# Performance work log

Hardware: AMD Instinct MI355X
Metric: run time of the kernel (lower is better)

Reference implementation:

```python
import jax, jax.numpy as jnp
import numpy as np

# static config matching init_kwargs / input_specs
SPATIAL = [(64, 64), (32, 32), (16, 16), (8, 8)]  # (H_l, W_l) per level
LEN = sum(h * w for h, w in SPATIAL)  # 5440
B, C, H, L, P = 4, 256, 8, 4, 4
DH = C // H
DFF = 1024
EPS = 1e-5


def layer_norm(x, g, b):
    m = x.mean(-1, keepdims=True)
    v = ((x - m) ** 2).mean(-1, keepdims=True)
    return (x - m) / jnp.sqrt(v + EPS) * g + b


def msda_core(value, sampling_locations, attn_weights):
    """Multi-scale deformable attention core (bilinear sample + weighted sum).
    value: [B, Len, H, DH]; sampling_locations: [B, Lq, H, L, P, 2] in [0,1];
    attn_weights: [B, Lq, H, L, P]. Returns [B, Lq, C].
    Matches grid_sample(bilinear, align_corners=False, padding_mode='zeros')."""
    Bn, Lq = sampling_locations.shape[0], sampling_locations.shape[1]
    out = jnp.zeros((Bn, H, Lq, DH), value.dtype)
    start = 0
    for l, (Hl, Wl) in enumerate(SPATIAL):
        vl = value[:, start:start + Hl * Wl]          # [B, Hl*Wl, H, DH]
        start += Hl * Wl
        vl = vl.transpose(0, 2, 1, 3)                  # [B, H, Hl*Wl, DH]
        loc = sampling_locations[:, :, :, l].transpose(0, 2, 1, 3, 4)  # [B,H,Lq,P,2]
        # align_corners=False: pixel = loc * size - 0.5
        px = loc[..., 0] * Wl - 0.5
        py = loc[..., 1] * Hl - 0.5
        x0 = jnp.floor(px); y0 = jnp.floor(py)
        wx1 = px - x0; wy1 = py - y0
        x0i = x0.astype(jnp.int32); y0i = y0.astype(jnp.int32)
        samp = jnp.zeros((Bn, H, Lq, P, DH), value.dtype)
        for dx, dy in ((0, 0), (1, 0), (0, 1), (1, 1)):
            ix = x0i + dx; iy = y0i + dy
            w = (wx1 if dx else 1.0 - wx1) * (wy1 if dy else 1.0 - wy1)
            valid = (ix >= 0) & (ix < Wl) & (iy >= 0) & (iy < Hl)
            idx = jnp.clip(iy, 0, Hl - 1) * Wl + jnp.clip(ix, 0, Wl - 1)  # [B,H,Lq,P]
            g = jnp.take_along_axis(vl, idx.reshape(Bn, H, -1)[..., None], axis=2)
            g = g.reshape(Bn, H, Lq, P, DH)
            samp = samp + g * (w * valid)[..., None]
        aw = attn_weights[:, :, :, l].transpose(0, 2, 1, 3)  # [B,H,Lq,P]
        out = out + (samp * aw[..., None]).sum(3)
    return out.transpose(0, 2, 1, 3).reshape(Bn, Lq, C)


def setup_inputs() -> dict:
    key = jax.random.key(0)
    ks = jax.random.split(key, 20)
    inp = {
        'src': jax.random.normal(ks[0], (B, LEN, C), jnp.float32),
        'pos': jax.random.normal(ks[1], (B, LEN, C), jnp.float32),
        'reference_points': jax.random.uniform(ks[2], (B, LEN, L, 2), jnp.float32),
        'spatial_shapes': jnp.array(SPATIAL, dtype=jnp.int32),
        'level_start_index': jnp.array(np.cumsum([0] + [h * w for h, w in SPATIAL[:-1]]), dtype=jnp.int32),
        'valid_ratios': jnp.ones((B, L, 2), jnp.float32),
        # MSDeformAttn params
        'w_off': jax.random.normal(ks[3], (C, H * L * P * 2), jnp.float32) * 0.01,
        'b_off': jax.random.normal(ks[4], (H * L * P * 2,), jnp.float32) * 0.5,
        'w_attn': jax.random.normal(ks[5], (C, H * L * P), jnp.float32) * 0.05,
        'b_attn': jnp.zeros((H * L * P,), jnp.float32),
        'w_val': jax.random.normal(ks[6], (C, C), jnp.float32) * 0.05,
        'b_val': jnp.zeros((C,), jnp.float32),
        'w_out': jax.random.normal(ks[7], (C, C), jnp.float32) * 0.05,
        'b_out': jnp.zeros((C,), jnp.float32),
        # norm1 + FFN + norm2 params
        'g1': jnp.ones((C,), jnp.float32), 'be1': jnp.zeros((C,), jnp.float32),
        'w1': jax.random.normal(ks[8], (C, DFF), jnp.float32) * 0.05,
        'b1': jnp.zeros((DFF,), jnp.float32),
        'w2': jax.random.normal(ks[9], (DFF, C), jnp.float32) * 0.05,
        'b2': jnp.zeros((C,), jnp.float32),
        'g2': jnp.ones((C,), jnp.float32), 'be2': jnp.zeros((C,), jnp.float32),
    }
    return inp


def reference(src, pos, reference_points, spatial_shapes, level_start_index, valid_ratios,
              w_off, b_off, w_attn, b_attn, w_val, b_val, w_out, b_out,
              g1, be1, w1, b1, w2, b2, g2, be2):
    Bn, Lq, _ = src.shape
    q = src + pos  # with_pos_embed
    off = (q @ w_off + b_off).reshape(Bn, Lq, H, L, P, 2)
    aw = jax.nn.softmax((q @ w_attn + b_attn).reshape(Bn, Lq, H, L * P), axis=-1)
    aw = aw.reshape(Bn, Lq, H, L, P)
    # offset normalizer is (W_l, H_l) per level
    norm = jnp.array([[w, h] for h, w in SPATIAL], dtype=src.dtype)  # [L, 2]
    loc = reference_points[:, :, None, :, None, :] + off / norm[None, None, None, :, None, :]
    value = (src @ w_val + b_val).reshape(Bn, Lq, H, DH)  # padding_mask is None
    attn_out = msda_core(value, loc, aw) @ w_out + b_out
    x = layer_norm(src + attn_out, g1, be1)
    ffn = jax.nn.relu(x @ w1 + b1) @ w2 + b2
    return layer_norm(x + ffn, g2, be2)
```

## Files before the change

### kernel.cpp

```cpp
#include <hip/hip_runtime.h>
#include <hip/hip_fp16.h>
#include <math.h>

#define LEN   5440
#define NTOK  21760
#define DFF   1024
#define LEPS  1e-5f

typedef __attribute__((ext_vector_type(8))) _Float16 f16x8;
typedef __attribute__((ext_vector_type(4))) float f32x4;

__device__ __forceinline__ float4 f4_add(float4 a, float4 b) {
    return make_float4(a.x + b.x, a.y + b.y, a.z + b.z, a.w + b.w);
}

__device__ __forceinline__ __half2 u2h2(unsigned u) {
    union { unsigned u; __half2 h; } c; c.u = u; return c.h;
}

__device__ __forceinline__ int swz8(int lin, int nwg) {
    const int q = nwg >> 3, r = nwg & 7;
    const int x = lin & 7, j = lin >> 3;
    return (x < r ? x * (q + 1) : r * (q + 1) + (x - r) * q) + j;
}

__global__ __launch_bounds__(256) void pack_k(const float* __restrict__ w_off,
                                              const float* __restrict__ w_attn,
                                              const float* __restrict__ w_val,
                                              const float* __restrict__ b_off,
                                              const float* __restrict__ b_attn,
                                              const float* __restrict__ b_val,
                                              const float* __restrict__ w_out,
                                              const float* __restrict__ w1,
                                              const float* __restrict__ w2,
                                              __half* __restrict__ WcatT,
                                              __half* __restrict__ woutT,
                                              __half* __restrict__ w1T,
                                              __half* __restrict__ w2T,
                                              float* __restrict__ bcat) {
    const int i = blockIdx.x * 256 + threadIdx.x;
    if (i < 163840) {
        const int c = i >> 8, k = i & 255;
        float v;
        if (c < 256)      v = w_off[k * 256 + c];
        else if (c < 384) v = w_attn[k * 128 + (c - 256)];
        else              v = w_val[k * 256 + (c - 384)];
        WcatT[i] = __float2half(v);
    } else if (i < 229376) {
        const int j = i - 163840, c = j >> 8, k = j & 255;
        woutT[j] = __float2half(w_out[k * 256 + c]);
    } else if (i < 491520) {
        const int j = i - 229376, c = j >> 8, k = j & 255;
        w1T[j] = __float2half(w1[k * 1024 + c]);
    } else if (i < 753664) {
        const int j = i - 491520, c = j >> 10, k = j & 1023;
        w2T[j] = __float2half(w2[k * 256 + c]);
    }
    if (i < 640) {
        bcat[i] = (i < 256) ? b_off[i] : (i < 384) ? b_attn[i - 256] : b_val[i - 384];
    }
}

template <bool AF32, int OMODE>
__global__ __launch_bounds__(256) void hgemm_k(const void* __restrict__ Ap,
                                               const float* __restrict__ A2f,
                                               const __half* __restrict__ Bt,
                                               const float* __restrict__ bias,
                                               float* __restrict__ Cf,
                                               __half* __restrict__ Ch,
                                               int NnF, int NnH, int K, int colSwitch) {
    __shared__ __half As[128][40];
    __shared__ __half Bs[128][40];
    const int nbx = gridDim.x;
    const int nwg = nbx * gridDim.y;
    const int tile = swz8(blockIdx.y * nbx + blockIdx.x, nwg);
    const int bx = tile % nbx, by = tile / nbx;

    const int tid = threadIdx.x;
    const int lane = tid & 63;
    const int wave = tid >> 6;
    const int wr = (wave >> 1) * 64;
    const int wc = (wave & 1) * 64;
    const bool useA2 = AF32 && (bx * 128 < colSwitch);

    const int srow = tid >> 1;
    const int sk = (tid & 1) * 16;

    const __half* Brow   = Bt + (size_t)(bx * 128 + srow) * K + sk;
    const float*  Afrow  = AF32 ? ((const float*)Ap + (size_t)(by * 128 + srow) * K + sk) : nullptr;
    const float*  Pfrow  = useA2 ? (A2f + (size_t)(by * 128 + srow) * K + sk) : nullptr;
    const __half* Ahrow  = AF32 ? nullptr : ((const __half*)Ap + (size_t)(by * 128 + srow) * K + sk);

    f32x4 acc[4][4];
#pragma unroll
    for (int m = 0; m < 4; ++m)
#pragma unroll
        for (int n = 0; n < 4; ++n) acc[m][n] = (f32x4){0.f, 0.f, 0.f, 0.f};

    const int fr = lane & 15;
    const int fk = (lane >> 4) * 8;

    uint4 a0, a1, b0, b1;
    float4 ra0, ra1, ra2, ra3, rp0, rp1, rp2, rp3;

    if (AF32) {
        ra0 = *(const float4*)(Afrow + 0);
        ra1 = *(const float4*)(Afrow + 4);
        ra2 = *(const float4*)(Afrow + 8);
        ra3 = *(const float4*)(Afrow + 12);
        if (useA2) {
            rp0 = *(const float4*)(Pfrow + 0);
            rp1 = *(const float4*)(Pfrow + 4);
            rp2 = *(const float4*)(Pfrow + 8);
            rp3 = *(const float4*)(Pfrow + 12);
        }
    } else {
        a0 = *(const uint4*)(Ahrow + 0);
        a1 = *(const uint4*)(Ahrow + 8);
    }
    b0 = *(const uint4*)(Brow + 0);
    b1 = *(const uint4*)(Brow + 8);

    for (int k0 = 0; k0 < K; k0 += 32) {
        __syncthreads();
        if (AF32) {
            float4 f0 = ra0, f1 = ra1, f2 = ra2, f3 = ra3;
            if (useA2) {
                f0 = f4_add(f0, rp0);
                f1 = f4_add(f1, rp1);
                f2 = f4_add(f2, rp2);
                f3 = f4_add(f3, rp3);
            }
            union { __half2 h[8]; uint4 u[2]; } cv;
            cv.h[0] = __floats2half2_rn(f0.x, f0.y);
            cv.h[1] = __floats2half2_rn(f0.z, f0.w);
            cv.h[2] = __floats2half2_rn(f1.x, f1.y);
            cv.h[3] = __floats2half2_rn(f1.z, f1.w);
            cv.h[4] = __floats2half2_rn(f2.x, f2.y);
            cv.h[5] = __floats2half2_rn(f2.z, f2.w);
            cv.h[6] = __floats2half2_rn(f3.x, f3.y);
            cv.h[7] = __floats2half2_rn(f3.z, f3.w);
            a0 = cv.u[0];
            a1 = cv.u[1];
        }
        *(uint4*)&As[srow][sk]     = a0;
        *(uint4*)&As[srow][sk + 8] = a1;
        *(uint4*)&Bs[srow][sk]     = b0;
        *(uint4*)&Bs[srow][sk + 8] = b1;
        __syncthreads();

        const int kn = k0 + 32;
        if (kn < K) {
            if (AF32) {
                ra0 = *(const float4*)(Afrow + kn + 0);
                ra1 = *(const float4*)(Afrow + kn + 4);
                ra2 = *(const float4*)(Afrow + kn + 8);
                ra3 = *(const float4*)(Afrow + kn + 12);
                if (useA2) {
                    rp0 = *(const float4*)(Pfrow + kn + 0);
                    rp1 = *(const float4*)(Pfrow + kn + 4);
                    rp2 = *(const float4*)(Pfrow + kn + 8);
                    rp3 = *(const float4*)(Pfrow + kn + 12);
                }
            } else {
                a0 = *(const uint4*)(Ahrow + kn + 0);
                a1 = *(const uint4*)(Ahrow + kn + 8);
            }
            b0 = *(const uint4*)(Brow + kn + 0);
            b1 = *(const uint4*)(Brow + kn + 8);
        }

        f16x8 af[4], bf[4];
#pragma unroll
        for (int m = 0; m < 4; ++m) af[m] = *(const f16x8*)&As[wr + m * 16 + fr][fk];
#pragma unroll
        for (int n = 0; n < 4; ++n) bf[n] = *(const f16x8*)&Bs[wc + n * 16 + fr][fk];
#pragma unroll
        for (int m = 0; m < 4; ++m)
#pragma unroll
            for (int n = 0; n < 4; ++n)
                acc[m][n] = __builtin_amdgcn_mfma_f32_16x16x32_f16(af[m], bf[n], acc[m][n], 0, 0, 0);
    }

    const int rowb = by * 128 + wr + (lane >> 4) * 4;
    const int colb = bx * 128 + wc + fr;
    float bn[4];
#pragma unroll
    for (int n = 0; n < 4; ++n) bn[n] = bias[colb + n * 16];
    const bool vhalf = (OMODE == 2) || (OMODE == 3 && bx * 128 >= colSwitch);
    const int colh = (OMODE == 3) ? (colb - colSwitch) : colb;
#pragma unroll
    for (int m = 0; m < 4; ++m) {
#pragma unroll
        for (int r = 0; r < 4; ++r) {
            const int row = rowb + m * 16 + r;
#pragma unroll
            for (int n = 0; n < 4; ++n) {
                float v = acc[m][n][r] + bn[n];
                if (OMODE == 2) v = fmaxf(v, 0.f);
                if (vhalf) Ch[(size_t)row * NnH + colh + n * 16] = __float2half(v);
                else       Cf[(size_t)row * NnF + colb + n * 16] = v;
            }
        }
    }
}

__global__ __launch_bounds__(256) void msda_kernel(const float* __restrict__ C1a,
                                                   const __half* __restrict__ Vh,
                                                   const float* __restrict__ refp,
                                                   __half* __restrict__ out) {
    __shared__ int      sOff[16][17][4];
    __shared__ unsigned sWh[16][17][4];
    const int tid = threadIdx.x;
    const int gi = tid >> 4;
    const int si = tid & 15;
    const int tile = swz8(blockIdx.x, gridDim.x);
    const int n = tile * 2 + (gi >> 3);
    const int h = gi & 7;
    const int b = n / LEN;

    {
        const int l = si >> 2, p = si & 3;
        const float lg = C1a[(size_t)n * 384 + 256 + h * 16 + si];
        float mx = lg;
#pragma unroll
        for (int m = 1; m < 16; m <<= 1) mx = fmaxf(mx, __shfl_xor(mx, m, 16));
        const float e = __expf(lg - mx);
        float sum = e;
#pragma unroll
        for (int m = 1; m < 16; m <<= 1) sum += __shfl_xor(sum, m, 16);
        const float aw = e / sum;

        const int Wi[4] = {64, 32, 16, 8};
        const int st[4] = {0, 4096, 5120, 5376};
        const int W = Wi[l];
        const float Wf = (float)W;
        const float rx = refp[((size_t)n * 4 + l) * 2 + 0];
        const float ry = refp[((size_t)n * 4 + l) * 2 + 1];
        const float2 oxy = *(const float2*)&C1a[(size_t)n * 384 + (((h * 4 + l) * 4 + p) * 2)];
        const float lx = rx + oxy.x / Wf;
        const float ly = ry + oxy.y / Wf;
        const float px = lx * Wf - 0.5f;
        const float py = ly * Wf - 0.5f;
        const float x0f = floorf(px), y0f = floorf(py);
        const float wx1 = px - x0f, wy1 = py - y0f;
        const int x0 = (int)x0f, y0 = (int)y0f;
#pragma unroll
        for (int c = 0; c < 4; ++c) {
            const int dx = c & 1, dy = c >> 1;
            const int ix = x0 + dx, iy = y0 + dy;
            const float wgt = (dx ? wx1 : 1.f - wx1) * (dy ? wy1 : 1.f - wy1);
            const bool valid = (ix >= 0) && (ix < W) && (iy >= 0) && (iy < W);
            const int ixc = min(max(ix, 0), W - 1);
            const int iyc = min(max(iy, 0), W - 1);
            const int pos = st[l] + iyc * W + ixc;
            sOff[gi][si][c] = ((b * LEN + pos) << 9) + (h << 6);
            const float wa = valid ? (aw * wgt) : 0.f;
            const unsigned wu = (unsigned)__half_as_ushort(__float2half_rn(wa));
            sWh[gi][si][c] = wu | (wu << 16);
        }
    }
    __syncthreads();

    const int cbyte = (si & 3) * 16;
    const int sb = (si >> 2) * 4;
    __half2 acc0 = u2h2(0), acc1 = u2h2(0), acc2 = u2h2(0), acc3 = u2h2(0);
    const char* Vb = (const char*)Vh;
#pragma unroll
    for (int t = 0; t < 4; ++t) {
        const int s = sb + t;
        const int4  off = *(const int4*)&sOff[gi][s][0];
        const uint4 wq  = *(const uint4*)&sWh[gi][s][0];
        union { uint4 u; __half2 h2[4]; } v0, v1, v2, v3;
        v0.u = *(const uint4*)(Vb + off.x + cbyte);
        v1.u = *(const uint4*)(Vb + off.y + cbyte);
        v2.u = *(const uint4*)(Vb + off.z + cbyte);
        v3.u = *(const uint4*)(Vb + off.w + cbyte);
        const __half2 w0 = u2h2(wq.x), w1 = u2h2(wq.y), w2 = u2h2(wq.z), w3 = u2h2(wq.w);
        acc0 = __hfma2(v0.h2[0], w0, acc0);
        acc1 = __hfma2(v0.h2[1], w0, acc1);
        acc2 = __hfma2(v0.h2[2], w0, acc2);
        acc3 = __hfma2(v0.h2[3], w0, acc3);
        acc0 = __hfma2(v1.h2[0], w1, acc0);
        acc1 = __hfma2(v1.h2[1], w1, acc1);
        acc2 = __hfma2(v1.h2[2], w1, acc2);
        acc3 = __hfma2(v1.h2[3], w1, acc3);
        acc0 = __hfma2(v2.h2[0], w2, acc0);
        acc1 = __hfma2(v2.h2[1], w2, acc1);
        acc2 = __hfma2(v2.h2[2], w2, acc2);
        acc3 = __hfma2(v2.h2[3], w2, acc3);
        acc0 = __hfma2(v3.h2[0], w3, acc0);
        acc1 = __hfma2(v3.h2[1], w3, acc1);
        acc2 = __hfma2(v3.h2[2], w3, acc2);
        acc3 = __hfma2(v3.h2[3], w3, acc3);
    }
    float f0 = __low2float(acc0), f1 = __high2float(acc0);
    float f2 = __low2float(acc1), f3 = __high2float(acc1);
    float f4 = __low2float(acc2), f5 = __high2float(acc2);
    float f6 = __low2float(acc3), f7 = __high2float(acc3);
#pragma unroll
    for (int m = 4; m <= 8; m <<= 1) {
        f0 += __shfl_xor(f0, m, 64);
        f1 += __shfl_xor(f1, m, 64);
        f2 += __shfl_xor(f2, m, 64);
        f3 += __shfl_xor(f3, m, 64);
        f4 += __shfl_xor(f4, m, 64);
        f5 += __shfl_xor(f5, m, 64);
        f6 += __shfl_xor(f6, m, 64);
        f7 += __shfl_xor(f7, m, 64);
    }
    if (si < 4) {
        union { __half2 h2[4]; uint4 u; } O;
        O.h2[0] = __floats2half2_rn(f0, f1);
        O.h2[1] = __floats2half2_rn(f2, f3);
        O.h2[2] = __floats2half2_rn(f4, f5);
        O.h2[3] = __floats2half2_rn(f6, f7);
        *(uint4*)&out[(size_t)n * 256 + h * 32 + si * 8] = O.u;
    }
}

template <bool WH>
__global__ __launch_bounds__(256) void ln_kernel(const float* __restrict__ Y,
                                                 const float* __restrict__ R,
                                                 const float* __restrict__ gm,
                                                 const float* __restrict__ bt,
                                                 float* __restrict__ O,
                                                 __half* __restrict__ OH) {
    const int wave = threadIdx.x >> 6, lane = threadIdx.x & 63;
    const int n = blockIdx.x * 4 + wave;
    const size_t base = (size_t)n * 256 + lane * 4;
    float4 y = *(const float4*)&Y[base];
    float4 r = *(const float4*)&R[base];
    float4 v = f4_add(y, r);
    float s = v.x + v.y + v.z + v.w;
#pragma unroll
    for (int m = 1; m < 64; m <<= 1) s += __shfl_xor(s, m, 64);
    const float mean = s * (1.f / 256.f);
    const float dx = v.x - mean, dy = v.y - mean, dz = v.z - mean, dw = v.w - mean;
    float ss = dx * dx + dy * dy + dz * dz + dw * dw;
#pragma unroll
    for (int m = 1; m < 64; m <<= 1) ss += __shfl_xor(ss, m, 64);
    const float rstd = rsqrtf(ss * (1.f / 256.f) + LEPS);
    const float4 g4 = *(const float4*)&gm[lane * 4];
    const float4 b4 = *(const float4*)&bt[lane * 4];
    float4 o;
    o.x = dx * rstd * g4.x + b4.x;
    o.y = dy * rstd * g4.y + b4.y;
    o.z = dz * rstd * g4.z + b4.z;
    o.w = dw * rstd * g4.w + b4.w;
    *(float4*)&O[base] = o;
    if (WH) {
        union { __half2 h[2]; uint2 u; } Hh;
        Hh.h[0] = __floats2half2_rn(o.x, o.y);
        Hh.h[1] = __floats2half2_rn(o.z, o.w);
        *(uint2*)&OH[base] = Hh.u;
    }
}

extern "C" void kernel_launch(void* const* d_in, const int* in_sizes, int n_in,
                              void* d_out, int out_size, void* d_ws, size_t ws_size,
                              hipStream_t stream) {
    const float* src   = (const float*)d_in[0];
    const float* pos   = (const float*)d_in[1];
    const float* refp  = (const float*)d_in[2];
    const float* w_off  = (const float*)d_in[6];
    const float* b_off  = (const float*)d_in[7];
    const float* w_attn = (const float*)d_in[8];
    const float* b_attn = (const float*)d_in[9];
    const float* w_val  = (const float*)d_in[10];
    const float* b_val  = (const float*)d_in[11];
    const float* w_out  = (const float*)d_in[12];
    const float* b_out  = (const float*)d_in[13];
    const float* g1     = (const float*)d_in[14];
    const float* be1    = (const float*)d_in[15];
    const float* w1     = (const float*)d_in[16];
    const float* b1     = (const float*)d_in[17];
    const float* w2     = (const float*)d_in[18];
    const float* b2     = (const float*)d_in[19];
    const float* g2     = (const float*)d_in[20];
    const float* be2    = (const float*)d_in[21];

    float* ws = (float*)d_ws;
    float*  C1a   = ws + 0;
    __half* Vh    = (__half*)(ws + 8355840);
    __half* msdah = (__half*)(ws + 11141120);
    float*  xbuf  = ws + 13926400;
    __half* xh    = (__half*)(ws + 19496960);
    __half* hh    = (__half*)(ws + 22282240);
    __half* WcatT = (__half*)(ws + 33423360);
    __half* woutT = (__half*)(ws + 33505280);
    __half* w1T   = (__half*)(ws + 33538048);
    __half* w2T   = (__half*)(ws + 33669120);
    float*  bcat  = ws + 33800192;
    float*  ybuf  = C1a;

    pack_k<<<2944, 256, 0, stream>>>(w_off, w_attn, w_val, b_off, b_attn, b_val,
                                     w_out, w1, w2, WcatT, woutT, w1T, w2T, bcat);

    hgemm_k<true, 3><<<dim3(5, 170), 256, 0, stream>>>(
        (const void*)src, pos, WcatT, bcat, C1a, Vh, 384, 256, 256, 384);

    msda_kernel<<<NTOK / 2, 256, 0, stream>>>(C1a, Vh, refp, msdah);

    hgemm_k<false, 0><<<dim3(2, 170), 256, 0, stream>>>(
        (const void*)msdah, nullptr, woutT, b_out, ybuf, nullptr, 256, 256, 256, 0);

    ln_kernel<true><<<NTOK / 4, 256, 0, stream>>>(ybuf, src, g1, be1, xbuf, xh);

    hgemm_k<false, 2><<<dim3(8, 170), 256, 0, stream>>>(
        (const void*)xh, nullptr, w1T, b1, nullptr, hh, 1024, 1024, 256, 0);

    hgemm_k<false, 0><<<dim3(2, 170), 256, 0, stream>>>(
        (const void*)hh, nullptr, w2T, b2, ybuf, nullptr, 256, 256, 1024, 0);

    ln_kernel<false><<<NTOK / 4, 256, 0, stream>>>(ybuf, xbuf, g2, be2, (float*)d_out, nullptr);
}
```

Measured before the change: 278.2 us.

## Double-buffer GEMM shared tiles and use 64-row tiles for N=256 GEMMs

The GEMM kernel now keeps two shared-memory buffers for A and B, so the next k-slice is stored while MFMAs run on the current one. This drops one of the two barriers per iteration. A BM template parameter adds a 64-row tile variant, used for the two GEMMs with 256 output columns. That doubles their grid to 680 workgroups to fill more CUs, at the cost of less reuse of B per tile and doubled LDS use.

```diff
diff --git a/kernel.cpp b/kernel.cpp
--- a/kernel.cpp
+++ b/kernel.cpp
@@ -61,7 +61,7 @@
     }
 }
 
-template <bool AF32, int OMODE>
+template <int BM, bool AF32, int OMODE>
 __global__ __launch_bounds__(256) void hgemm_k(const void* __restrict__ Ap,
                                                const float* __restrict__ A2f,
                                                const __half* __restrict__ Bt,
@@ -69,8 +69,9 @@
                                                float* __restrict__ Cf,
                                                __half* __restrict__ Ch,
                                                int NnF, int NnH, int K, int colSwitch) {
-    __shared__ __half As[128][40];
-    __shared__ __half Bs[128][40];
+    __shared__ __half As[2][BM][40];
+    __shared__ __half Bs[2][128][40];
+    constexpr int MR = (BM == 128) ? 4 : 2;
     const int nbx = gridDim.x;
     const int nwg = nbx * gridDim.y;
     const int tile = swz8(blockIdx.y * nbx + blockIdx.x, nwg);
@@ -79,21 +80,22 @@
     const int tid = threadIdx.x;
     const int lane = tid & 63;
     const int wave = tid >> 6;
-    const int wr = (wave >> 1) * 64;
+    const int wr = (BM == 128) ? (wave >> 1) * 64 : (wave >> 1) * 32;
     const int wc = (wave & 1) * 64;
     const bool useA2 = AF32 && (bx * 128 < colSwitch);
 
     const int srow = tid >> 1;
     const int sk = (tid & 1) * 16;
-
-    const __half* Brow   = Bt + (size_t)(bx * 128 + srow) * K + sk;
-    const float*  Afrow  = AF32 ? ((const float*)Ap + (size_t)(by * 128 + srow) * K + sk) : nullptr;
-    const float*  Pfrow  = useA2 ? (A2f + (size_t)(by * 128 + srow) * K + sk) : nullptr;
-    const __half* Ahrow  = AF32 ? nullptr : ((const __half*)Ap + (size_t)(by * 128 + srow) * K + sk);
-
-    f32x4 acc[4][4];
-#pragma unroll
-    for (int m = 0; m < 4; ++m)
+    const bool doA = (BM == 128) || (tid < 128);
+
+    const __half* Brow  = Bt + (size_t)(bx * 128 + srow) * K + sk;
+    const float*  Afrow = AF32 ? ((const float*)Ap + (size_t)(by * BM + srow) * K + sk) : nullptr;
+    const float*  Pfrow = useA2 ? (A2f + (size_t)(by * BM + srow) * K + sk) : nullptr;
+    const __half* Ahrow = AF32 ? nullptr : ((const __half*)Ap + (size_t)(by * BM + srow) * K + sk);
+
+    f32x4 acc[MR][4];
+#pragma unroll
+    for (int m = 0; m < MR; ++m)
 #pragma unroll
         for (int n = 0; n < 4; ++n) acc[m][n] = (f32x4){0.f, 0.f, 0.f, 0.f};
 
@@ -103,86 +105,90 @@
     uint4 a0, a1, b0, b1;
     float4 ra0, ra1, ra2, ra3, rp0, rp1, rp2, rp3;
 
-    if (AF32) {
-        ra0 = *(const float4*)(Afrow + 0);
-        ra1 = *(const float4*)(Afrow + 4);
-        ra2 = *(const float4*)(Afrow + 8);
-        ra3 = *(const float4*)(Afrow + 12);
-        if (useA2) {
-            rp0 = *(const float4*)(Pfrow + 0);
-            rp1 = *(const float4*)(Pfrow + 4);
-            rp2 = *(const float4*)(Pfrow + 8);
-            rp3 = *(const float4*)(Pfrow + 12);
-        }
-    } else {
-        a0 = *(const uint4*)(Ahrow + 0);
-        a1 = *(const uint4*)(Ahrow + 8);
-    }
-    b0 = *(const uint4*)(Brow + 0);
-    b1 = *(const uint4*)(Brow + 8);
-
+#define LOADQ(koff)                                                       \
+    do {                                                                  \
+        if (doA) {                                                        \
+            if (AF32) {                                                   \
+                ra0 = *(const float4*)(Afrow + (koff) + 0);               \
+                ra1 = *(const float4*)(Afrow + (koff) + 4);               \
+                ra2 = *(const float4*)(Afrow + (koff) + 8);               \
+                ra3 = *(const float4*)(Afrow + (koff) + 12);              \
+                if (useA2) {                                              \
+                    rp0 = *(const float4*)(Pfrow + (koff) + 0);           \
+                    rp1 = *(const float4*)(Pfrow + (koff) + 4);           \
+                    rp2 = *(const float4*)(Pfrow + (koff) + 8);           \
+                    rp3 = *(const float4*)(Pfrow + (koff) + 12);          \
+                }                                                         \
+            } else {                                                      \
+                a0 = *(const uint4*)(Ahrow + (koff) + 0);                 \
+                a1 = *(const uint4*)(Ahrow + (koff) + 8);                 \
+            }                                                             \
+        }                                                                 \
+        b0 = *(const uint4*)(Brow + (koff) + 0);                          \
+        b1 = *(const uint4*)(Brow + (koff) + 8);                          \
+    } while (0)
+
+#define STOREQ(buf)                                                       \
+    do {                                                                  \
+        if (doA) {                                                        \
+            if (AF32) {                                                   \
+                float4 f0 = ra0, f1 = ra1, f2 = ra2, f3 = ra3;            \
+                if (useA2) {                                              \
+                    f0 = f4_add(f0, rp0);                                 \
+                    f1 = f4_add(f1, rp1);                                 \
+                    f2 = f4_add(f2, rp2);                                 \
+                    f3 = f4_add(f3, rp3);                                 \
+                }                                                         \
+                union { __half2 h[8]; uint4 u[2]; } cv;                   \
+                cv.h[0] = __floats2half2_rn(f0.x, f0.y);                  \
+                cv.h[1] = __floats2half2_rn(f0.z, f0.w);                  \
+                cv.h[2] = __floats2half2_rn(f1.x, f1.y);                  \
+                cv.h[3] = __floats2half2_rn(f1.z, f1.w);                  \
+                cv.h[4] = __floats2half2_rn(f2.x, f2.y);                  \
+                cv.h[5] = __floats2half2_rn(f2.z, f2.w);                  \
+                cv.h[6] = __floats2half2_rn(f3.x, f3.y);                  \
+                cv.h[7] = __floats2half2_rn(f3.z, f3.w);                  \
+                a0 = cv.u[0];                                             \
+                a1 = cv.u[1];                                             \
+            }                                                             \
+            *(uint4*)&As[buf][srow][sk]     = a0;                         \
+            *(uint4*)&As[buf][srow][sk + 8] = a1;                         \
+        }                                                                 \
+        *(uint4*)&Bs[buf][srow][sk]     = b0;                             \
+        *(uint4*)&Bs[buf][srow][sk + 8] = b1;                             \
+    } while (0)
+
+    LOADQ(0);
+    STOREQ(0);
+    if (32 < K) LOADQ(32);
+    __syncthreads();
+
+    int cur = 0;
     for (int k0 = 0; k0 < K; k0 += 32) {
-        __syncthreads();
-        if (AF32) {
-            float4 f0 = ra0, f1 = ra1, f2 = ra2, f3 = ra3;
-            if (useA2) {
-                f0 = f4_add(f0, rp0);
-                f1 = f4_add(f1, rp1);
-                f2 = f4_add(f2, rp2);
-                f3 = f4_add(f3, rp3);
-            }
-            union { __half2 h[8]; uint4 u[2]; } cv;
-            cv.h[0] = __floats2half2_rn(f0.x, f0.y);
-            cv.h[1] = __floats2half2_rn(f0.z, f0.w);
-            cv.h[2] = __floats2half2_rn(f1.x, f1.y);
-            cv.h[3] = __floats2half2_rn(f1.z, f1.w);
-            cv.h[4] = __floats2half2_rn(f2.x, f2.y);
-            cv.h[5] = __floats2half2_rn(f2.z, f2.w);
-            cv.h[6] = __floats2half2_rn(f3.x, f3.y);
-            cv.h[7] = __floats2half2_rn(f3.z, f3.w);
-            a0 = cv.u[0];
-            a1 = cv.u[1];
-        }
-        *(uint4*)&As[srow][sk]     = a0;
-        *(uint4*)&As[srow][sk + 8] = a1;
-        *(uint4*)&Bs[srow][sk]     = b0;
-        *(uint4*)&Bs[srow][sk + 8] = b1;
-        __syncthreads();
-
-        const int kn = k0 + 32;
-        if (kn < K) {
-            if (AF32) {
-                ra0 = *(const float4*)(Afrow + kn + 0);
-                ra1 = *(const float4*)(Afrow + kn + 4);
-                ra2 = *(const float4*)(Afrow + kn + 8);
-                ra3 = *(const float4*)(Afrow + kn + 12);
-                if (useA2) {
-                    rp0 = *(const float4*)(Pfrow + kn + 0);
-                    rp1 = *(const float4*)(Pfrow + kn + 4);
-                    rp2 = *(const float4*)(Pfrow + kn + 8);
-                    rp3 = *(const float4*)(Pfrow + kn + 12);
-                }
-            } else {
-                a0 = *(const uint4*)(Ahrow + kn + 0);
-                a1 = *(const uint4*)(Ahrow + kn + 8);
-            }
-            b0 = *(const uint4*)(Brow + kn + 0);
-            b1 = *(const uint4*)(Brow + kn + 8);
-        }
-
-        f16x8 af[4], bf[4];
-#pragma unroll
-        for (int m = 0; m < 4; ++m) af[m] = *(const f16x8*)&As[wr + m * 16 + fr][fk];
-#pragma unroll
-        for (int n = 0; n < 4; ++n) bf[n] = *(const f16x8*)&Bs[wc + n * 16 + fr][fk];
-#pragma unroll
-        for (int m = 0; m < 4; ++m)
+        f16x8 af[MR], bf[4];
+#pragma unroll
+        for (int m = 0; m < MR; ++m) af[m] = *(const f16x8*)&As[cur][wr + m * 16 + fr][fk];
+#pragma unroll
+        for (int n = 0; n < 4; ++n) bf[n] = *(const f16x8*)&Bs[cur][wc + n * 16 + fr][fk];
+#pragma unroll
+        for (int m = 0; m < MR; ++m)
 #pragma unroll
             for (int n = 0; n < 4; ++n)
                 acc[m][n] = __builtin_amdgcn_mfma_f32_16x16x32_f16(af[m], bf[n], acc[m][n], 0, 0, 0);
-    }
-
-    const int rowb = by * 128 + wr + (lane >> 4) * 4;
+
+        const int kstore = k0 + 32;
+        if (kstore < K) {
+            STOREQ(cur ^ 1);
+            const int kiss = k0 + 64;
+            if (kiss < K) LOADQ(kiss);
+            __syncthreads();
+            cur ^= 1;
+        }
+    }
+#undef LOADQ
+#undef STOREQ
+
+    const int rowb = by * BM + wr + (lane >> 4) * 4;
     const int colb = bx * 128 + wc + fr;
     float bn[4];
 #pragma unroll
@@ -190,7 +196,7 @@
     const bool vhalf = (OMODE == 2) || (OMODE == 3 && bx * 128 >= colSwitch);
     const int colh = (OMODE == 3) ? (colb - colSwitch) : colb;
 #pragma unroll
-    for (int m = 0; m < 4; ++m) {
+    for (int m = 0; m < MR; ++m) {
 #pragma unroll
         for (int r = 0; r < 4; ++r) {
             const int row = rowb + m * 16 + r;
@@ -397,20 +403,20 @@
     pack_k<<<2944, 256, 0, stream>>>(w_off, w_attn, w_val, b_off, b_attn, b_val,
                                      w_out, w1, w2, WcatT, woutT, w1T, w2T, bcat);
 
-    hgemm_k<true, 3><<<dim3(5, 170), 256, 0, stream>>>(
+    hgemm_k<128, true, 3><<<dim3(5, 170), 256, 0, stream>>>(
         (const void*)src, pos, WcatT, bcat, C1a, Vh, 384, 256, 256, 384);
 
     msda_kernel<<<NTOK / 2, 256, 0, stream>>>(C1a, Vh, refp, msdah);
 
-    hgemm_k<false, 0><<<dim3(2, 170), 256, 0, stream>>>(
+    hgemm_k<64, false, 0><<<dim3(2, 340), 256, 0, stream>>>(
         (const void*)msdah, nullptr, woutT, b_out, ybuf, nullptr, 256, 256, 256, 0);
 
     ln_kernel<true><<<NTOK / 4, 256, 0, stream>>>(ybuf, src, g1, be1, xbuf, xh);
 
-    hgemm_k<false, 2><<<dim3(8, 170), 256, 0, stream>>>(
+    hgemm_k<128, false, 2><<<dim3(8, 170), 256, 0, stream>>>(
         (const void*)xh, nullptr, w1T, b1, nullptr, hh, 1024, 1024, 256, 0);
 
-    hgemm_k<false, 0><<<dim3(2, 170), 256, 0, stream>>>(
+    hgemm_k<64, false, 0><<<dim3(2, 340), 256, 0, stream>>>(
         (const void*)hh, nullptr, w2T, b2, ybuf, nullptr, 256, 256, 1024, 0);
 
     ln_kernel<false><<<NTOK / 4, 256, 0, stream>>>(ybuf, xbuf, g2, be2, (float*)d_out, nullptr);
```

After: 279.7 us. No clear change (+0.5%).

## Rewrite GEMM with direct global-to-LDS loads, 256-wide K chunks and swizzled LDS

Applied to the files above, without the earlier changes.

The GEMM kernel now loads whole 256-wide K chunks straight into shared memory with global_load_lds and an XOR-swizzled layout, replacing the per-32-K register staging loop. The fp32 src+pos conversion moves into a separate cvt_k pre-pass that writes half-precision copies. The smaller-N GEMMs use 64x64 tiles to launch more workgroups. The aim is to cut load instruction overhead and sync count and to raise occupancy. The cost is much larger LDS use (up to 128 KB per block for 128x128 tiles), no load/compute overlap inside a chunk, and an extra conversion pass.

```diff
diff --git a/kernel.cpp b/kernel.cpp
--- a/kernel.cpp
+++ b/kernel.cpp
@@ -16,6 +16,12 @@
 
 __device__ __forceinline__ __half2 u2h2(unsigned u) {
     union { unsigned u; __half2 h; } c; c.u = u; return c.h;
+}
+
+__device__ __forceinline__ void gload_lds16(const void* g, void* l) {
+    __builtin_amdgcn_global_load_lds(
+        (const __attribute__((address_space(1))) unsigned int*)g,
+        (__attribute__((address_space(3))) unsigned int*)l, 16, 0, 0);
 }
 
 __device__ __forceinline__ int swz8(int lin, int nwg) {
@@ -61,141 +67,109 @@
     }
 }
 
-template <bool AF32, int OMODE>
-__global__ __launch_bounds__(256) void hgemm_k(const void* __restrict__ Ap,
-                                               const float* __restrict__ A2f,
+__global__ __launch_bounds__(256) void cvt_k(const float* __restrict__ src,
+                                             const float* __restrict__ pos,
+                                             __half* __restrict__ qh,
+                                             __half* __restrict__ srch) {
+    const size_t i = (size_t)blockIdx.x * 256 + threadIdx.x;
+    float4 s = *(const float4*)&src[i * 4];
+    float4 p = *(const float4*)&pos[i * 4];
+    union { __half2 h[2]; uint2 u; } Q, S;
+    Q.h[0] = __floats2half2_rn(s.x + p.x, s.y + p.y);
+    Q.h[1] = __floats2half2_rn(s.z + p.z, s.w + p.w);
+    S.h[0] = __floats2half2_rn(s.x, s.y);
+    S.h[1] = __floats2half2_rn(s.z, s.w);
+    *(uint2*)&qh[i * 4]   = Q.u;
+    *(uint2*)&srch[i * 4] = S.u;
+}
+
+template <int BM, int BN, int OMODE>
+__global__ __launch_bounds__(256) void hgemm_k(const __half* __restrict__ Aq,
+                                               const __half* __restrict__ Av,
                                                const __half* __restrict__ Bt,
                                                const float* __restrict__ bias,
                                                float* __restrict__ Cf,
                                                __half* __restrict__ Ch,
                                                int NnF, int NnH, int K, int colSwitch) {
-    __shared__ __half As[128][40];
-    __shared__ __half Bs[128][40];
+    constexpr int KC = 256;
+    constexpr int MR = BM / 32;
+    constexpr int NR = BN / 32;
+    __shared__ __half As[BM][KC];
+    __shared__ __half Bs[BN][KC];
+
     const int nbx = gridDim.x;
-    const int nwg = nbx * gridDim.y;
-    const int tile = swz8(blockIdx.y * nbx + blockIdx.x, nwg);
+    const int tile = swz8(blockIdx.y * nbx + blockIdx.x, nbx * gridDim.y);
     const int bx = tile % nbx, by = tile / nbx;
 
     const int tid = threadIdx.x;
     const int lane = tid & 63;
     const int wave = tid >> 6;
-    const int wr = (wave >> 1) * 64;
-    const int wc = (wave & 1) * 64;
-    const bool useA2 = AF32 && (bx * 128 < colSwitch);
-
-    const int srow = tid >> 1;
-    const int sk = (tid & 1) * 16;
-
-    const __half* Brow   = Bt + (size_t)(bx * 128 + srow) * K + sk;
-    const float*  Afrow  = AF32 ? ((const float*)Ap + (size_t)(by * 128 + srow) * K + sk) : nullptr;
-    const float*  Pfrow  = useA2 ? (A2f + (size_t)(by * 128 + srow) * K + sk) : nullptr;
-    const __half* Ahrow  = AF32 ? nullptr : ((const __half*)Ap + (size_t)(by * 128 + srow) * K + sk);
-
-    f32x4 acc[4][4];
-#pragma unroll
-    for (int m = 0; m < 4; ++m)
-#pragma unroll
-        for (int n = 0; n < 4; ++n) acc[m][n] = (f32x4){0.f, 0.f, 0.f, 0.f};
+    const int wr = (wave >> 1) * (BM / 2);
+    const int wc = (wave & 1) * (BN / 2);
+
+    const __half* __restrict__ Ah = (bx * BN < colSwitch) ? Aq : Av;
+
+    const int rl = lane >> 5, ck = lane & 31;
+    const int xm = (2 * wave + rl) & 7;
+    const int colx = ((ck ^ xm) << 3);
+    const __half* Ap = Ah + (size_t)(by * BM + 2 * wave + rl) * K + colx;
+    const __half* Bp = Bt + (size_t)(bx * BN + 2 * wave + rl) * K + colx;
 
     const int fr = lane & 15;
-    const int fk = (lane >> 4) * 8;
-
-    uint4 a0, a1, b0, b1;
-    float4 ra0, ra1, ra2, ra3, rp0, rp1, rp2, rp3;
-
-    if (AF32) {
-        ra0 = *(const float4*)(Afrow + 0);
-        ra1 = *(const float4*)(Afrow + 4);
-        ra2 = *(const float4*)(Afrow + 8);
-        ra3 = *(const float4*)(Afrow + 12);
-        if (useA2) {
-            rp0 = *(const float4*)(Pfrow + 0);
-            rp1 = *(const float4*)(Pfrow + 4);
-            rp2 = *(const float4*)(Pfrow + 8);
-            rp3 = *(const float4*)(Pfrow + 12);
+    const int hi = lane >> 4;
+    const int xr = fr & 7;
+
+    f32x4 acc[MR][NR];
+#pragma unroll
+    for (int m = 0; m < MR; ++m)
+#pragma unroll
+        for (int n = 0; n < NR; ++n) acc[m][n] = (f32x4){0.f, 0.f, 0.f, 0.f};
+
+    for (int kc = 0; kc < K; kc += KC) {
+        if (kc) __syncthreads();
+#pragma unroll
+        for (int j = 0; j < BM / 8; ++j)
+            gload_lds16(Ap + ((size_t)(8 * j) * K + kc), &As[2 * wave + 8 * j][0]);
+#pragma unroll
+        for (int j = 0; j < BN / 8; ++j)
+            gload_lds16(Bp + ((size_t)(8 * j) * K + kc), &Bs[2 * wave + 8 * j][0]);
+        __syncthreads();
+
+        const char* Ab = (const char*)&As[0][0];
+        const char* Bb = (const char*)&Bs[0][0];
+#pragma unroll
+        for (int kk = 0; kk < KC / 32; ++kk) {
+            const int cb = (kk << 2) + hi;
+            const int co = ((cb ^ xr) << 4);
+            f16x8 af[MR], bf[NR];
+#pragma unroll
+            for (int m = 0; m < MR; ++m)
+                af[m] = *(const f16x8*)(Ab + (wr + m * 16 + fr) * (KC * 2) + co);
+#pragma unroll
+            for (int n = 0; n < NR; ++n)
+                bf[n] = *(const f16x8*)(Bb + (wc + n * 16 + fr) * (KC * 2) + co);
+#pragma unroll
+            for (int m = 0; m < MR; ++m)
+#pragma unroll
+                for (int n = 0; n < NR; ++n)
+                    acc[m][n] = __builtin_amdgcn_mfma_f32_16x16x32_f16(af[m], bf[n], acc[m][n], 0, 0, 0);
         }
-    } else {
-        a0 = *(const uint4*)(Ahrow + 0);
-        a1 = *(const uint4*)(Ahrow + 8);
-    }
-    b0 = *(const uint4*)(Brow + 0);
-    b1 = *(const uint4*)(Brow + 8);
-
-    for (int k0 = 0; k0 < K; k0 += 32) {
-        __syncthreads();
-        if (AF32) {
-            float4 f0 = ra0, f1 = ra1, f2 = ra2, f3 = ra3;
-            if (useA2) {
-                f0 = f4_add(f0, rp0);
-                f1 = f4_add(f1, rp1);
-                f2 = f4_add(f2, rp2);
-                f3 = f4_add(f3, rp3);
-            }
-            union { __half2 h[8]; uint4 u[2]; } cv;
-            cv.h[0] = __floats2half2_rn(f0.x, f0.y);
-            cv.h[1] = __floats2half2_rn(f0.z, f0.w);
-            cv.h[2] = __floats2half2_rn(f1.x, f1.y);
-            cv.h[3] = __floats2half2_rn(f1.z, f1.w);
-            cv.h[4] = __floats2half2_rn(f2.x, f2.y);
-            cv.h[5] = __floats2half2_rn(f2.z, f2.w);
-            cv.h[6] = __floats2half2_rn(f3.x, f3.y);
-            cv.h[7] = __floats2half2_rn(f3.z, f3.w);
-            a0 = cv.u[0];
-            a1 = cv.u[1];
-        }
-        *(uint4*)&As[srow][sk]     = a0;
-        *(uint4*)&As[srow][sk + 8] = a1;
-        *(uint4*)&Bs[srow][sk]     = b0;
-        *(uint4*)&Bs[srow][sk + 8] = b1;
-        __syncthreads();
-
-        const int kn = k0 + 32;
-        if (kn < K) {
-            if (AF32) {
-                ra0 = *(const float4*)(Afrow + kn + 0);
-                ra1 = *(const float4*)(Afrow + kn + 4);
-                ra2 = *(const float4*)(Afrow + kn + 8);
-                ra3 = *(const float4*)(Afrow + kn + 12);
-                if (useA2) {
-                    rp0 = *(const float4*)(Pfrow + kn + 0);
-                    rp1 = *(const float4*)(Pfrow + kn + 4);
-                    rp2 = *(const float4*)(Pfrow + kn + 8);
-                    rp3 = *(const float4*)(Pfrow + kn + 12);
-                }
-            } else {
-                a0 = *(const uint4*)(Ahrow + kn + 0);
-                a1 = *(const uint4*)(Ahrow + kn + 8);
-            }
-            b0 = *(const uint4*)(Brow + kn + 0);
-            b1 = *(const uint4*)(Brow + kn + 8);
-        }
-
-        f16x8 af[4], bf[4];
-#pragma unroll
-        for (int m = 0; m < 4; ++m) af[m] = *(const f16x8*)&As[wr + m * 16 + fr][fk];
-#pragma unroll
-        for (int n = 0; n < 4; ++n) bf[n] = *(const f16x8*)&Bs[wc + n * 16 + fr][fk];
-#pragma unroll
-        for (int m = 0; m < 4; ++m)
-#pragma unroll
-            for (int n = 0; n < 4; ++n)
-                acc[m][n] = __builtin_amdgcn_mfma_f32_16x16x32_f16(af[m], bf[n], acc[m][n], 0, 0, 0);
-    }
-
-    const int rowb = by * 128 + wr + (lane >> 4) * 4;
-    const int colb = bx * 128 + wc + fr;
-    float bn[4];
-#pragma unroll
-    for (int n = 0; n < 4; ++n) bn[n] = bias[colb + n * 16];
-    const bool vhalf = (OMODE == 2) || (OMODE == 3 && bx * 128 >= colSwitch);
+    }
+
+    const int rowb = by * BM + wr + hi * 4;
+    const int colb = bx * BN + wc + fr;
+    float bn[NR];
+#pragma unroll
+    for (int n = 0; n < NR; ++n) bn[n] = bias[colb + n * 16];
+    const bool vhalf = (OMODE == 2) || (OMODE == 3 && bx * BN >= colSwitch);
     const int colh = (OMODE == 3) ? (colb - colSwitch) : colb;
 #pragma unroll
-    for (int m = 0; m < 4; ++m) {
+    for (int m = 0; m < MR; ++m) {
 #pragma unroll
         for (int r = 0; r < 4; ++r) {
             const int row = rowb + m * 16 + r;
 #pragma unroll
-            for (int n = 0; n < 4; ++n) {
+            for (int n = 0; n < NR; ++n) {
                 float v = acc[m][n][r] + bn[n];
                 if (OMODE == 2) v = fmaxf(v, 0.f);
                 if (vhalf) Ch[(size_t)row * NnH + colh + n * 16] = __float2half(v);
@@ -387,31 +361,34 @@
     float*  xbuf  = ws + 13926400;
     __half* xh    = (__half*)(ws + 19496960);
     __half* hh    = (__half*)(ws + 22282240);
-    __half* WcatT = (__half*)(ws + 33423360);
-    __half* woutT = (__half*)(ws + 33505280);
-    __half* w1T   = (__half*)(ws + 33538048);
-    __half* w2T   = (__half*)(ws + 33669120);
-    float*  bcat  = ws + 33800192;
+    __half* qh    = (__half*)(ws + 33423360);
+    __half* srch  = (__half*)(ws + 36208640);
+    __half* WcatT = (__half*)(ws + 38993920);
+    __half* woutT = (__half*)(ws + 39075840);
+    __half* w1T   = (__half*)(ws + 39108608);
+    __half* w2T   = (__half*)(ws + 39239680);
+    float*  bcat  = ws + 39370752;
     float*  ybuf  = C1a;
 
     pack_k<<<2944, 256, 0, stream>>>(w_off, w_attn, w_val, b_off, b_attn, b_val,
                                      w_out, w1, w2, WcatT, woutT, w1T, w2T, bcat);
-
-    hgemm_k<true, 3><<<dim3(5, 170), 256, 0, stream>>>(
-        (const void*)src, pos, WcatT, bcat, C1a, Vh, 384, 256, 256, 384);
+    cvt_k<<<5440, 256, 0, stream>>>(src, pos, qh, srch);
+
+    hgemm_k<128, 128, 3><<<dim3(5, 170), 256, 0, stream>>>(
+        qh, srch, WcatT, bcat, C1a, Vh, 384, 256, 256, 384);
 
     msda_kernel<<<NTOK / 2, 256, 0, stream>>>(C1a, Vh, refp, msdah);
 
-    hgemm_k<false, 0><<<dim3(2, 170), 256, 0, stream>>>(
-        (const void*)msdah, nullptr, woutT, b_out, ybuf, nullptr, 256, 256, 256, 0);
+    hgemm_k<64, 64, 0><<<dim3(4, 340), 256, 0, stream>>>(
+        msdah, msdah, woutT, b_out, ybuf, nullptr, 256, 256, 256, 1 << 30);
 
     ln_kernel<true><<<NTOK / 4, 256, 0, stream>>>(ybuf, src, g1, be1, xbuf, xh);
 
-    hgemm_k<false, 2><<<dim3(8, 170), 256, 0, stream>>>(
-        (const void*)xh, nullptr, w1T, b1, nullptr, hh, 1024, 1024, 256, 0);
-
-    hgemm_k<false, 0><<<dim3(2, 170), 256, 0, stream>>>(
-        (const void*)hh, nullptr, w2T, b2, ybuf, nullptr, 256, 256, 1024, 0);
+    hgemm_k<128, 128, 2><<<dim3(8, 170), 256, 0, stream>>>(
+        xh, xh, w1T, b1, nullptr, hh, 1024, 1024, 256, 1 << 30);
+
+    hgemm_k<64, 64, 0><<<dim3(4, 340), 256, 0, stream>>>(
+        hh, hh, w2T, b2, ybuf, nullptr, 256, 256, 1024, 1 << 30);
 
     ln_kernel<false><<<NTOK / 4, 256, 0, stream>>>(ybuf, xbuf, g2, be2, (float*)d_out, nullptr);
 }
```

Measured after the change: 285.9 us. +2.8%, slower.
